# Optimization experiments

Measured on AMD Instinct MI355X. Metric: run time of the kernel, lower is better.

## Reference

```python
import jax, jax.numpy as jnp
import numpy as np

B, S, E, H = 4, 2048, 1024, 16
D = E // H  # head_dim = 64


def setup_inputs() -> dict:
    key = jax.random.key(0)
    k1, k2, k3 = jax.random.split(key, 3)
    x = jax.random.normal(k1, (B, S, E), dtype=jnp.float32)
    w_attn = jax.random.normal(k2, (E, 3 * E), dtype=jnp.float32) * (E ** -0.5)
    b_attn = jnp.zeros((3 * E,), dtype=jnp.float32)
    w_out = jax.random.normal(k3, (E, E), dtype=jnp.float32) * (E ** -0.5)
    b_out = jnp.zeros((E,), dtype=jnp.float32)
    return {"x": x, "w_attn": w_attn, "b_attn": b_attn, "w_out": w_out, "b_out": b_out}


def reference(x, w_attn, b_attn, w_out, b_out):
    b, s, e = x.shape
    qkv = x @ w_attn + b_attn                      # [b, s, 3e]
    q, k, v = jnp.split(qkv, 3, axis=2)
    q = q.reshape(b, s, H, D)
    k = k.reshape(b, s, H, D)
    v = v.reshape(b, s, H, D)
    energy = jnp.einsum('nqhd,nkhd->nhqk', q, k)   # [b, H, s, s]
    causal = jnp.tril(jnp.ones((s, s), dtype=bool))
    energy = jnp.where(causal, energy, -jnp.inf)
    scale = jnp.sqrt(jnp.float32(D))
    attn = jax.nn.softmax(energy / scale, axis=-1)  # dropout_rate=0.0 -> identity
    out = jnp.einsum('nhql,nlhd->nqhd', attn, v).reshape(b, s, e)
    return out @ w_out + b_out
```

## Files before the change

### kernel.cpp

```cpp
#include <hip/hip_runtime.h>

typedef short bf16x8 __attribute__((ext_vector_type(8)));
typedef float f32x4 __attribute__((ext_vector_type(4)));
typedef float f32x16 __attribute__((ext_vector_type(16)));
typedef float float4v __attribute__((ext_vector_type(4)));
typedef short short4v __attribute__((ext_vector_type(4)));
typedef unsigned uint2v __attribute__((ext_vector_type(2)));
typedef unsigned uint4v __attribute__((ext_vector_type(4)));

#define B_ 4
#define S_ 2048
#define E_ 1024
#define H_ 16
#define D_ 64
#define M_ (B_*S_)
#define N1_ (3*E_)

__device__ inline short f2bs(float f) {
    unsigned u = __builtin_bit_cast(unsigned, f);
    unsigned r = u + 0x7fffu + ((u >> 16) & 1u);
    return (short)(r >> 16);
}
__device__ inline float exp2a(float x) {
    float r; asm("v_exp_f32 %0, %1" : "=v"(r) : "v"(x)); return r;
}
__device__ inline unsigned cvtpk(float a, float b) {
    unsigned r; asm("v_cvt_pk_bf16_f32 %0, %1, %2" : "=v"(r) : "v"(a), "v"(b)); return r;
}

__device__ inline const __attribute__((address_space(1))) void* gas(const void* p) {
    return (const __attribute__((address_space(1))) void*)p;
}
__device__ inline __attribute__((address_space(3))) void* las(void* p) {
    return (__attribute__((address_space(3))) void*)p;
}

__global__ void convert_f32_bf16(const float* __restrict__ in, short* __restrict__ out, int n) {
    int tid = blockIdx.x * blockDim.x + threadIdx.x;
    int stride = gridDim.x * blockDim.x;
    for (int i = tid * 4; i < n; i += stride * 4) {
        float4v v = *(const float4v*)&in[i];
        short4v o;
        o[0] = f2bs(v[0]); o[1] = f2bs(v[1]); o[2] = f2bs(v[2]); o[3] = f2bs(v[3]);
        *(short4v*)&out[i] = o;
    }
}

__global__ void transpose_convert(const float* __restrict__ in, short* __restrict__ out,
                                  int rows, int cols) {
    __shared__ float t[32][33];
    int bx = blockIdx.x * 32;
    int by = blockIdx.y * 32;
    int tx = threadIdx.x, ty = threadIdx.y;
#pragma unroll
    for (int i = 0; i < 4; ++i)
        t[ty + i * 8][tx] = in[(size_t)(by + ty + i * 8) * cols + bx + tx];
    __syncthreads();
#pragma unroll
    for (int i = 0; i < 4; ++i)
        out[(size_t)(bx + ty + i * 8) * rows + by + tx] = f2bs(t[tx][ty + i * 8]);
}

#define MFMA16(Q) \
    _Pragma("unroll") for (int mf = 0; mf < 2; ++mf) \
    _Pragma("unroll") for (int nf = 0; nf < 4; ++nf) { \
        acc[(Q)*2+mf][nf] = __builtin_amdgcn_mfma_f32_16x16x32_bf16(af[mf][0], bfrag[nf][0], acc[(Q)*2+mf][nf], 0, 0, 0); \
        acc[(Q)*2+mf][nf] = __builtin_amdgcn_mfma_f32_16x16x32_bf16(af[mf][1], bfrag[nf][1], acc[(Q)*2+mf][nf], 0, 0, 0); \
    }

#define PHASE(Q, STAGE_STMT, WAITV) do { \
    bf16x8 af[2][2]; \
    _Pragma("unroll") for (int mf = 0; mf < 2; ++mf) \
    _Pragma("unroll") for (int ks = 0; ks < 2; ++ks) { \
        int r = (Q)*32 + mf*16 + li; \
        af[mf][ks] = *(const bf16x8*)(lA + r*128 + ((ks*64 + g*16) ^ ((r & 7) << 4))); \
    } \
    STAGE_STMT; \
    __builtin_amdgcn_s_barrier(); \
    asm volatile("s_waitcnt lgkmcnt(0)" ::: "memory"); \
    __builtin_amdgcn_sched_barrier(0); \
    __builtin_amdgcn_s_setprio(1); \
    MFMA16(Q); \
    __builtin_amdgcn_s_setprio(0); \
    WAITV; \
    __builtin_amdgcn_s_barrier(); \
} while (0)

#define VMW(n) asm volatile("s_waitcnt vmcnt(" #n ")" ::: "memory")
#define NOP_ ((void)0)

__global__ __launch_bounds__(512, 2) void gemm256_qkv(
    const short* __restrict__ A, const short* __restrict__ Bt,
    const float* __restrict__ bias,
    short* __restrict__ Qb, short* __restrict__ Kb, short* __restrict__ Vt) {
    __shared__ __attribute__((aligned(16))) short lds[2][2][2][8192];
    const int tid = threadIdx.x;
    const int lane = tid & 63;
    const int wid = tid >> 6;
    const int li = lane & 15, g = lane >> 4;
    const int wr = wid >> 2, wc = wid & 3;
    const int Kdim = E_;
    const int NT = Kdim >> 6;

    const int id = blockIdx.x;
    const int swz = (id & 7) * 48 + (id >> 3);
    const int bx = swz % 12, by = swz / 12;
    const int row0 = by * 256, col0 = bx * 256;

    const int rstage = wid * 8 + (lane >> 3);
    const int cstage = (((lane & 7) ^ ((lane >> 3) & 7)) << 4);

    auto stageA = [&](int buf, int kt, int seg) {
#pragma unroll
        for (int h = 0; h < 2; ++h) {
            const char* src = (const char*)A +
                ((size_t)(row0 + h * 128 + seg * 64 + rstage) * Kdim + kt * 64) * 2 + cstage;
            char* dst = (char*)&lds[buf][0][h][0] + seg * 8192 + wid * 1024;
            __builtin_amdgcn_global_load_lds(gas(src), las(dst), 16, 0, 0);
        }
    };
    auto stageB = [&](int buf, int kt, int h) {
#pragma unroll
        for (int seg = 0; seg < 2; ++seg) {
            const char* src = (const char*)Bt +
                ((size_t)(col0 + h * 128 + seg * 64 + rstage) * Kdim + kt * 64) * 2 + cstage;
            char* dst = (char*)&lds[buf][1][h][0] + seg * 8192 + wid * 1024;
            __builtin_amdgcn_global_load_lds(gas(src), las(dst), 16, 0, 0);
        }
    };

    f32x4 acc[8][4];
#pragma unroll
    for (int m = 0; m < 8; ++m)
#pragma unroll
        for (int n = 0; n < 4; ++n) acc[m][n] = (f32x4){0.f, 0.f, 0.f, 0.f};

    stageB(0, 0, 0);
    stageB(0, 0, 1);
    stageA(0, 0, 0);
    stageA(0, 0, 1);
    asm volatile("s_waitcnt vmcnt(0)" ::: "memory");
    __syncthreads();

    const int bc = (wc & 1) * 64;
    for (int t = 0; t < NT; ++t) {
        const int cur = t & 1;
        const int nb = cur ^ 1;
        const int tn = t + 1;
        const bool st = (tn < NT);
        const char* lA = (const char*)&lds[cur][0][wr][0];
        const char* lB = (const char*)&lds[cur][1][wc >> 1][0];

        bf16x8 bfrag[4][2];
#pragma unroll
        for (int nf = 0; nf < 4; ++nf)
#pragma unroll
            for (int ks = 0; ks < 2; ++ks) {
                int r = bc + nf * 16 + li;
                bfrag[nf][ks] = *(const bf16x8*)(lB + r * 128 + ((ks * 64 + g * 16) ^ ((r & 7) << 4)));
            }
        if (st) {
            PHASE(0, stageB(nb, tn, 0), NOP_);
            PHASE(1, stageB(nb, tn, 1), VMW(4));
            PHASE(2, stageA(nb, tn, 0), NOP_);
            PHASE(3, stageA(nb, tn, 1), VMW(2));
        } else {
            PHASE(0, NOP_, NOP_);
            PHASE(1, NOP_, VMW(0));
            PHASE(2, NOP_, NOP_);
            PHASE(3, NOP_, NOP_);
        }
    }

    if (col0 < 2048) {
        short* Dst = (col0 < 1024) ? Qb : Kb;
#pragma unroll
        for (int nf = 0; nf < 4; ++nf) {
            int ncolg = col0 + wc * 64 + nf * 16 + li;
            float bv = bias[ncolg];
            int ncol = ncolg & 1023;
#pragma unroll
            for (int mi = 0; mi < 8; ++mi) {
                int rbase = row0 + wr * 128 + mi * 16 + 4 * g;
#pragma unroll
                for (int j = 0; j < 4; ++j)
                    Dst[(size_t)(rbase + j) * E_ + ncol] = f2bs(acc[mi][nf][j] + bv);
            }
        }
    } else {
#pragma unroll
        for (int nf = 0; nf < 4; ++nf) {
            int ncolg = col0 + wc * 64 + nf * 16 + li;
            float bv = bias[ncolg];
            int rem = ncolg & 1023;
            int h = rem >> 6, d = rem & 63;
#pragma unroll
            for (int mi = 0; mi < 8; ++mi) {
                int s0 = row0 + wr * 128 + mi * 16 + 4 * g;
                int bb2 = s0 >> 11;
                int ss = s0 & 2047;
                uint2v p;
                p[0] = cvtpk(acc[mi][nf][0] + bv, acc[mi][nf][1] + bv);
                p[1] = cvtpk(acc[mi][nf][2] + bv, acc[mi][nf][3] + bv);
                *(uint2v*)&Vt[((size_t)(bb2 * H_ + h) * D_ + d) * S_ + ss] = p;
            }
        }
    }
}

__global__ __launch_bounds__(256, 2) void gemm_bt_out(
    const short* __restrict__ A, const short* __restrict__ Bt,
    const float* __restrict__ bias, float* __restrict__ Cf,
    int Kdim, int Ndim) {
    __shared__ __attribute__((aligned(16))) short As[128 * 32];
    __shared__ __attribute__((aligned(16))) short Bs[128 * 32];
    const int lane = threadIdx.x & 63;
    const int wv = threadIdx.x >> 6;
    const int row0 = blockIdx.y * 128;
    const int col0 = blockIdx.x * 128;
    const int wr = (wv >> 1) * 64;
    const int wc = (wv & 1) * 64;
    const int li = lane & 15;
    const int g = lane >> 4;
    const int lr = lane >> 2;
    const int lk = (lane & 3) * 8;

    f32x4 acc[4][4];
#pragma unroll
    for (int m = 0; m < 4; ++m)
#pragma unroll
        for (int n = 0; n < 4; ++n) acc[m][n] = (f32x4){0.f, 0.f, 0.f, 0.f};

    for (int k0 = 0; k0 < Kdim; k0 += 32) {
#pragma unroll
        for (int i = 0; i < 2; ++i) {
            int cc = wv * 2 + i;
            const short* ga = A + (size_t)(row0 + cc * 16 + lr) * Kdim + k0 + lk;
            __builtin_amdgcn_global_load_lds(gas(ga), las(&As[cc * 512]), 16, 0, 0);
            const short* gb = Bt + (size_t)(col0 + cc * 16 + lr) * Kdim + k0 + lk;
            __builtin_amdgcn_global_load_lds(gas(gb), las(&Bs[cc * 512]), 16, 0, 0);
        }
        __syncthreads();
        bf16x8 af[4], bfr[4];
#pragma unroll
        for (int m = 0; m < 4; ++m) af[m] = *(const bf16x8*)&As[(wr + 16 * m + li) * 32 + g * 8];
#pragma unroll
        for (int n = 0; n < 4; ++n) bfr[n] = *(const bf16x8*)&Bs[(wc + 16 * n + li) * 32 + g * 8];
#pragma unroll
        for (int m = 0; m < 4; ++m)
#pragma unroll
            for (int n = 0; n < 4; ++n)
                acc[m][n] = __builtin_amdgcn_mfma_f32_16x16x32_bf16(af[m], bfr[n], acc[m][n], 0, 0, 0);
        __syncthreads();
    }

#pragma unroll
    for (int n = 0; n < 4; ++n) {
        int ncol = col0 + wc + 16 * n + li;
        float bv = bias[ncol];
#pragma unroll
        for (int m = 0; m < 4; ++m) {
            int rbase = row0 + wr + 16 * m + 4 * g;
#pragma unroll
            for (int j = 0; j < 4; ++j)
                Cf[(size_t)(rbase + j) * Ndim + ncol] = acc[m][n][j] + bv;
        }
    }
}

__global__ __launch_bounds__(256, 4) void attn_kernel(
    const short* __restrict__ Qb, const short* __restrict__ Kb,
    const short* __restrict__ Vt, short* __restrict__ Ob) {
    __shared__ __attribute__((aligned(16))) short Kl[4096];
    __shared__ __attribute__((aligned(16))) short Vl[4096];
    const int lane = threadIdx.x & 63;
    const int wv = threadIdx.x >> 6;
    const int l31 = lane & 31;
    const int hi = lane >> 5;
    const int id = blockIdx.x;
    const int xcd = id & 7;
    const int r_ = id >> 3;
    const int qt = 15 - (r_ >> 3);
    const int bh = xcd * 8 + (r_ & 7);
    const int bb = bh >> 4, hh = bh & 15;
    const short* Qh = Qb + (size_t)bb * (S_ * E_) + hh * 64;
    const short* Kh = Kb + (size_t)bb * (S_ * E_) + hh * 64;
    const short* Vh = Vt + (size_t)bh * (D_ * S_);
    const float CEXP = 0.18033688011112042f;

    const int rstage = wv * 8 + (lane >> 3);
    const int cstage = (((lane & 7) ^ ((lane >> 3) & 7)) << 4);

    const int q0w = qt * 128 + wv * 32;
    const int q = q0w + l31;

    bf16x8 qf[4];
#pragma unroll
    for (int c = 0; c < 4; ++c)
        qf[c] = *(const bf16x8*)&Qh[(size_t)q * E_ + c * 16 + hi * 8];

    f32x16 acc[2];
#pragma unroll
    for (int d = 0; d < 2; ++d)
#pragma unroll
        for (int r = 0; r < 16; ++r) acc[d][r] = 0.f;
    float m = -3e38f, mC = 0.f, l = 0.f;

    const int nw = (q0w + 95) >> 6;
    const int nt = (qt * 128 + 191) >> 6;

    for (int it = 0; it < nt; ++it) {
        const int kt0 = it * 64;
#pragma unroll
        for (int half = 0; half < 2; ++half) {
            const char* gk = (const char*)(Kh + (size_t)(kt0 + half * 32 + rstage) * E_) + cstage;
            __builtin_amdgcn_global_load_lds(gas(gk), las((char*)Kl + half * 4096 + wv * 1024), 16, 0, 0);
            const char* gv = (const char*)Vh + (size_t)(half * 32 + rstage) * (S_ * 2) + (size_t)kt0 * 2 + cstage;
            __builtin_amdgcn_global_load_lds(gas(gv), las((char*)Vl + half * 4096 + wv * 1024), 16, 0, 0);
        }
        __syncthreads();
        if (it < nw) {
            f32x16 sc0, sc1;
#pragma unroll
            for (int r = 0; r < 16; ++r) { sc0[r] = 0.f; sc1[r] = 0.f; }
#pragma unroll
            for (int c = 0; c < 4; ++c) {
                const int r0 = l31, r1 = 32 + l31;
                bf16x8 kf0 = *(const bf16x8*)((const char*)Kl + r0 * 128 +
                                              ((c * 32 + hi * 16) ^ ((r0 & 7) << 4)));
                bf16x8 kf1 = *(const bf16x8*)((const char*)Kl + r1 * 128 +
                                              ((c * 32 + hi * 16) ^ ((r1 & 7) << 4)));
                sc0 = __builtin_amdgcn_mfma_f32_32x32x16_bf16(kf0, qf[c], sc0, 0, 0, 0);
                sc1 = __builtin_amdgcn_mfma_f32_32x32x16_bf16(kf1, qf[c], sc1, 0, 0, 0);
            }
            if (kt0 + 63 > q0w) {
                const int kb = kt0 + 4 * hi;
#pragma unroll
                for (int r = 0; r < 16; ++r) {
                    int key = kb + (r & 3) + 8 * (r >> 2);
                    sc0[r] = (key > q) ? -3e38f : sc0[r];
                    sc1[r] = (key + 32 > q) ? -3e38f : sc1[r];
                }
            }
            float tmx[8];
#pragma unroll
            for (int r = 0; r < 8; ++r)
                tmx[r] = fmaxf(fmaxf(sc0[2 * r], sc0[2 * r + 1]),
                               fmaxf(sc1[2 * r], sc1[2 * r + 1]));
            float tm = fmaxf(fmaxf(fmaxf(tmx[0], tmx[1]), fmaxf(tmx[2], tmx[3])),
                             fmaxf(fmaxf(tmx[4], tmx[5]), fmaxf(tmx[6], tmx[7])));
            tm = fmaxf(tm, __shfl_xor(tm, 32, 64));
            bool need = (tm > m + 16.0f);
            if (__ballot((int)need) != 0ull) {
                float mn = fmaxf(m, tm);
                float sf = exp2a((m - mn) * CEXP);
                m = mn; mC = mn * CEXP;
                l *= sf;
#pragma unroll
                for (int d = 0; d < 2; ++d)
#pragma unroll
                    for (int r = 0; r < 16; ++r) acc[d][r] *= sf;
            }
#pragma unroll
            for (int r = 0; r < 16; ++r) {
                sc0[r] = exp2a(fmaf(sc0[r], CEXP, -mC));
                sc1[r] = exp2a(fmaf(sc1[r], CEXP, -mC));
            }
            float s0 = 0.f, s1 = 0.f;
#pragma unroll
            for (int r = 0; r < 8; ++r) {
                s0 += sc0[2 * r] + sc0[2 * r + 1];
                s1 += sc1[2 * r] + sc1[2 * r + 1];
            }
            float ls = s0 + s1;
            ls += __shfl_xor(ls, 32, 64);
            l += ls;
            const bool lo = (hi == 0);
            bf16x8 pf[4];
#pragma unroll
            for (int s = 0; s < 2; ++s) {
                const f32x16& p = s ? sc1 : sc0;
                unsigned W0 = cvtpk(p[0], p[1]),   W1 = cvtpk(p[2], p[3]);
                unsigned W2 = cvtpk(p[4], p[5]),   W3 = cvtpk(p[6], p[7]);
                unsigned W4 = cvtpk(p[8], p[9]),   W5 = cvtpk(p[10], p[11]);
                unsigned W6 = cvtpk(p[12], p[13]), W7 = cvtpk(p[14], p[15]);
                unsigned xW0 = __shfl_xor(W0, 32, 64), xW1 = __shfl_xor(W1, 32, 64);
                unsigned xW2 = __shfl_xor(W2, 32, 64), xW3 = __shfl_xor(W3, 32, 64);
                unsigned xW4 = __shfl_xor(W4, 32, 64), xW5 = __shfl_xor(W5, 32, 64);
                unsigned xW6 = __shfl_xor(W6, 32, 64), xW7 = __shfl_xor(W7, 32, 64);
                uint4v u1, u2;
                u1[0] = lo ? W0 : xW2;  u1[1] = lo ? W1 : xW3;
                u1[2] = lo ? xW0 : W2;  u1[3] = lo ? xW1 : W3;
                u2[0] = lo ? W4 : xW6;  u2[1] = lo ? W5 : xW7;
                u2[2] = lo ? xW4 : W6;  u2[3] = lo ? xW5 : W7;
                pf[s * 2] = __builtin_bit_cast(bf16x8, u1);
                pf[s * 2 + 1] = __builtin_bit_cast(bf16x8, u2);
            }
#pragma unroll
            for (int db = 0; db < 2; ++db) {
                const int row = db * 32 + l31;
                const int rsw = (row & 7) << 4;
                const char* vrow = (const char*)Vl + row * 128;
                bf16x8 v0 = *(const bf16x8*)(vrow + ((hi * 16) ^ rsw));
                bf16x8 v1 = *(const bf16x8*)(vrow + ((32 + hi * 16) ^ rsw));
                bf16x8 v2 = *(const bf16x8*)(vrow + ((64 + hi * 16) ^ rsw));
                bf16x8 v3 = *(const bf16x8*)(vrow + ((96 + hi * 16) ^ rsw));
                acc[db] = __builtin_amdgcn_mfma_f32_32x32x16_bf16(v0, pf[0], acc[db], 0, 0, 0);
                acc[db] = __builtin_amdgcn_mfma_f32_32x32x16_bf16(v1, pf[1], acc[db], 0, 0, 0);
                acc[db] = __builtin_amdgcn_mfma_f32_32x32x16_bf16(v2, pf[2], acc[db], 0, 0, 0);
                acc[db] = __builtin_amdgcn_mfma_f32_32x32x16_bf16(v3, pf[3], acc[db], 0, 0, 0);
            }
        }
        __syncthreads();
    }

    float rl = __builtin_amdgcn_rcpf(l);
    short* orow = Ob + ((size_t)(bb * S_ + q)) * E_ + hh * 64;
#pragma unroll
    for (int db = 0; db < 2; ++db)
#pragma unroll
        for (int rb = 0; rb < 4; ++rb) {
            uint2v pk;
            pk[0] = cvtpk(acc[db][rb * 4 + 0] * rl, acc[db][rb * 4 + 1] * rl);
            pk[1] = cvtpk(acc[db][rb * 4 + 2] * rl, acc[db][rb * 4 + 3] * rl);
            *(uint2v*)&orow[db * 32 + rb * 8 + hi * 4] = pk;
        }
}

extern "C" void kernel_launch(void* const* d_in, const int* in_sizes, int n_in,
                              void* d_out, int out_size, void* d_ws, size_t ws_size,
                              hipStream_t stream) {
    const float* x      = (const float*)d_in[0];
    const float* w_attn = (const float*)d_in[1];
    const float* b_attn = (const float*)d_in[2];
    const float* w_out  = (const float*)d_in[3];
    const float* b_out  = (const float*)d_in[4];
    float* out = (float*)d_out;

    char* ws = (char*)d_ws;
    short* Xbf  = (short*)(ws);
    short* Wat  = (short*)(ws + (16ull << 20));
    short* Wot  = (short*)(ws + (22ull << 20));
    short* Qb   = (short*)(ws + (24ull << 20));
    short* Kb   = (short*)(ws + (40ull << 20));
    short* Vt   = (short*)(ws + (56ull << 20));
    short* Obuf = Xbf;

    convert_f32_bf16<<<2048, 256, 0, stream>>>(x, Xbf, M_ * E_);
    transpose_convert<<<dim3(N1_ / 32, E_ / 32), dim3(32, 8), 0, stream>>>(w_attn, Wat, E_, N1_);
    transpose_convert<<<dim3(E_ / 32, E_ / 32), dim3(32, 8), 0, stream>>>(w_out, Wot, E_, E_);

    gemm256_qkv<<<384, 512, 0, stream>>>(Xbf, Wat, b_attn, Qb, Kb, Vt);

    attn_kernel<<<1024, 256, 0, stream>>>(Qb, Kb, Vt, Obuf);

    gemm_bt_out<<<dim3(E_ / 128, M_ / 128), 256, 0, stream>>>(
        Obuf, Wot, b_out, out, E_, E_);
}
```

Measured before the change: 177.0 us.

## Narrow QKV GEMM tiles to 256x128 and double-buffer K/V in attention

The QKV projection GEMM now uses 256x128 output tiles, launching 768 blocks instead of 384 and halving the B-tile LDS footprint and the accumulator registers per thread. The loads are regrouped across the four pipeline phases to match. The attention kernel now double-buffers its K and V LDS tiles, prefetching the next key block while the current one is computed, to hide global load latency. The trade-offs are more LDS in attention, which may limit occupancy, and lower arithmetic intensity per GEMM block.

Measured after the change: 192.3 us. +8.6%, slower.

```diff
diff --git a/kernel.cpp b/kernel.cpp
--- a/kernel.cpp
+++ b/kernel.cpp
@@ -61,9 +61,9 @@
         out[(size_t)(bx + ty + i * 8) * rows + by + tx] = f2bs(t[tx][ty + i * 8]);
 }
 
-#define MFMA16(Q) \
+#define MFMA8(Q) \
     _Pragma("unroll") for (int mf = 0; mf < 2; ++mf) \
-    _Pragma("unroll") for (int nf = 0; nf < 4; ++nf) { \
+    _Pragma("unroll") for (int nf = 0; nf < 2; ++nf) { \
         acc[(Q)*2+mf][nf] = __builtin_amdgcn_mfma_f32_16x16x32_bf16(af[mf][0], bfrag[nf][0], acc[(Q)*2+mf][nf], 0, 0, 0); \
         acc[(Q)*2+mf][nf] = __builtin_amdgcn_mfma_f32_16x16x32_bf16(af[mf][1], bfrag[nf][1], acc[(Q)*2+mf][nf], 0, 0, 0); \
     }
@@ -80,7 +80,7 @@
     asm volatile("s_waitcnt lgkmcnt(0)" ::: "memory"); \
     __builtin_amdgcn_sched_barrier(0); \
     __builtin_amdgcn_s_setprio(1); \
-    MFMA16(Q); \
+    MFMA8(Q); \
     __builtin_amdgcn_s_setprio(0); \
     WAITV; \
     __builtin_amdgcn_s_barrier(); \
@@ -89,11 +89,12 @@
 #define VMW(n) asm volatile("s_waitcnt vmcnt(" #n ")" ::: "memory")
 #define NOP_ ((void)0)
 
-__global__ __launch_bounds__(512, 2) void gemm256_qkv(
+__global__ __launch_bounds__(512, 2) void gemm_qkv(
     const short* __restrict__ A, const short* __restrict__ Bt,
     const float* __restrict__ bias,
     short* __restrict__ Qb, short* __restrict__ Kb, short* __restrict__ Vt) {
-    __shared__ __attribute__((aligned(16))) short lds[2][2][2][8192];
+    __shared__ __attribute__((aligned(16))) short ldsA[2][2][2][4096];
+    __shared__ __attribute__((aligned(16))) short ldsB[2][8192];
     const int tid = threadIdx.x;
     const int lane = tid & 63;
     const int wid = tid >> 6;
@@ -103,9 +104,9 @@
     const int NT = Kdim >> 6;
 
     const int id = blockIdx.x;
-    const int swz = (id & 7) * 48 + (id >> 3);
-    const int bx = swz % 12, by = swz / 12;
-    const int row0 = by * 256, col0 = bx * 256;
+    const int swz = (id & 7) * 96 + (id >> 3);
+    const int bx = swz % 24, by = swz / 24;
+    const int row0 = by * 256, col0 = bx * 128;
 
     const int rstage = wid * 8 + (lane >> 3);
     const int cstage = (((lane & 7) ^ ((lane >> 3) & 7)) << 4);
@@ -115,55 +116,53 @@
         for (int h = 0; h < 2; ++h) {
             const char* src = (const char*)A +
                 ((size_t)(row0 + h * 128 + seg * 64 + rstage) * Kdim + kt * 64) * 2 + cstage;
-            char* dst = (char*)&lds[buf][0][h][0] + seg * 8192 + wid * 1024;
+            char* dst = (char*)&ldsA[buf][h][seg][0] + wid * 1024;
             __builtin_amdgcn_global_load_lds(gas(src), las(dst), 16, 0, 0);
         }
     };
-    auto stageB = [&](int buf, int kt, int h) {
-#pragma unroll
-        for (int seg = 0; seg < 2; ++seg) {
+    auto stageB = [&](int buf, int kt) {
+#pragma unroll
+        for (int i = 0; i < 2; ++i) {
             const char* src = (const char*)Bt +
-                ((size_t)(col0 + h * 128 + seg * 64 + rstage) * Kdim + kt * 64) * 2 + cstage;
-            char* dst = (char*)&lds[buf][1][h][0] + seg * 8192 + wid * 1024;
+                ((size_t)(col0 + i * 64 + rstage) * Kdim + kt * 64) * 2 + cstage;
+            char* dst = (char*)&ldsB[buf][0] + i * 8192 + wid * 1024;
             __builtin_amdgcn_global_load_lds(gas(src), las(dst), 16, 0, 0);
         }
     };
 
-    f32x4 acc[8][4];
+    f32x4 acc[8][2];
 #pragma unroll
     for (int m = 0; m < 8; ++m)
 #pragma unroll
-        for (int n = 0; n < 4; ++n) acc[m][n] = (f32x4){0.f, 0.f, 0.f, 0.f};
-
-    stageB(0, 0, 0);
-    stageB(0, 0, 1);
+        for (int n = 0; n < 2; ++n) acc[m][n] = (f32x4){0.f, 0.f, 0.f, 0.f};
+
+    stageB(0, 0);
     stageA(0, 0, 0);
     stageA(0, 0, 1);
     asm volatile("s_waitcnt vmcnt(0)" ::: "memory");
     __syncthreads();
 
-    const int bc = (wc & 1) * 64;
     for (int t = 0; t < NT; ++t) {
         const int cur = t & 1;
         const int nb = cur ^ 1;
         const int tn = t + 1;
         const bool st = (tn < NT);
-        const char* lA = (const char*)&lds[cur][0][wr][0];
-        const char* lB = (const char*)&lds[cur][1][wc >> 1][0];
-
-        bf16x8 bfrag[4][2];
-#pragma unroll
-        for (int nf = 0; nf < 4; ++nf)
+        const char* lA = (const char*)&ldsA[cur][wr][0][0];
+        const char* lB = (const char*)&ldsB[cur][0];
+
+        bf16x8 bfrag[2][2];
+#pragma unroll
+        for (int nf = 0; nf < 2; ++nf)
 #pragma unroll
             for (int ks = 0; ks < 2; ++ks) {
-                int r = bc + nf * 16 + li;
+                int r = wc * 32 + nf * 16 + li;
                 bfrag[nf][ks] = *(const bf16x8*)(lB + r * 128 + ((ks * 64 + g * 16) ^ ((r & 7) << 4)));
             }
         if (st) {
-            PHASE(0, stageB(nb, tn, 0), NOP_);
-            PHASE(1, stageB(nb, tn, 1), VMW(4));
-            PHASE(2, stageA(nb, tn, 0), NOP_);
-            PHASE(3, stageA(nb, tn, 1), VMW(2));
+            PHASE(0, stageB(nb, tn), NOP_);
+            PHASE(1, stageA(nb, tn, 0), VMW(4));
+            PHASE(2, stageA(nb, tn, 1), NOP_);
+            PHASE(3, NOP_, VMW(2));
         } else {
             PHASE(0, NOP_, NOP_);
             PHASE(1, NOP_, VMW(0));
@@ -175,8 +174,8 @@
     if (col0 < 2048) {
         short* Dst = (col0 < 1024) ? Qb : Kb;
 #pragma unroll
-        for (int nf = 0; nf < 4; ++nf) {
-            int ncolg = col0 + wc * 64 + nf * 16 + li;
+        for (int nf = 0; nf < 2; ++nf) {
+            int ncolg = col0 + wc * 32 + nf * 16 + li;
             float bv = bias[ncolg];
             int ncol = ncolg & 1023;
 #pragma unroll
@@ -189,8 +188,8 @@
         }
     } else {
 #pragma unroll
-        for (int nf = 0; nf < 4; ++nf) {
-            int ncolg = col0 + wc * 64 + nf * 16 + li;
+        for (int nf = 0; nf < 2; ++nf) {
+            int ncolg = col0 + wc * 32 + nf * 16 + li;
             float bv = bias[ncolg];
             int rem = ncolg & 1023;
             int h = rem >> 6, d = rem & 63;
@@ -271,8 +270,8 @@
 __global__ __launch_bounds__(256, 4) void attn_kernel(
     const short* __restrict__ Qb, const short* __restrict__ Kb,
     const short* __restrict__ Vt, short* __restrict__ Ob) {
-    __shared__ __attribute__((aligned(16))) short Kl[4096];
-    __shared__ __attribute__((aligned(16))) short Vl[4096];
+    __shared__ __attribute__((aligned(16))) short Kl[2][4096];
+    __shared__ __attribute__((aligned(16))) short Vl[2][4096];
     const int lane = threadIdx.x & 63;
     const int wv = threadIdx.x >> 6;
     const int l31 = lane & 31;
@@ -309,27 +308,35 @@
     const int nw = (q0w + 95) >> 6;
     const int nt = (qt * 128 + 191) >> 6;
 
-    for (int it = 0; it < nt; ++it) {
+    auto stage = [&](int it, int buf) {
         const int kt0 = it * 64;
 #pragma unroll
         for (int half = 0; half < 2; ++half) {
             const char* gk = (const char*)(Kh + (size_t)(kt0 + half * 32 + rstage) * E_) + cstage;
-            __builtin_amdgcn_global_load_lds(gas(gk), las((char*)Kl + half * 4096 + wv * 1024), 16, 0, 0);
+            __builtin_amdgcn_global_load_lds(gas(gk), las((char*)&Kl[buf][0] + half * 4096 + wv * 1024), 16, 0, 0);
             const char* gv = (const char*)Vh + (size_t)(half * 32 + rstage) * (S_ * 2) + (size_t)kt0 * 2 + cstage;
-            __builtin_amdgcn_global_load_lds(gas(gv), las((char*)Vl + half * 4096 + wv * 1024), 16, 0, 0);
-        }
-        __syncthreads();
+            __builtin_amdgcn_global_load_lds(gas(gv), las((char*)&Vl[buf][0] + half * 4096 + wv * 1024), 16, 0, 0);
+        }
+    };
+
+    stage(0, 0);
+    __syncthreads();
+
+    for (int it = 0; it < nt; ++it) {
+        const int buf = it & 1;
+        if (it + 1 < nt) stage(it + 1, buf ^ 1);
         if (it < nw) {
+            const int kt0 = it * 64;
+            const char* Kb_ = (const char*)&Kl[buf][0];
+            const char* Vb_ = (const char*)&Vl[buf][0];
             f32x16 sc0, sc1;
 #pragma unroll
             for (int r = 0; r < 16; ++r) { sc0[r] = 0.f; sc1[r] = 0.f; }
 #pragma unroll
             for (int c = 0; c < 4; ++c) {
                 const int r0 = l31, r1 = 32 + l31;
-                bf16x8 kf0 = *(const bf16x8*)((const char*)Kl + r0 * 128 +
-                                              ((c * 32 + hi * 16) ^ ((r0 & 7) << 4)));
-                bf16x8 kf1 = *(const bf16x8*)((const char*)Kl + r1 * 128 +
-                                              ((c * 32 + hi * 16) ^ ((r1 & 7) << 4)));
+                bf16x8 kf0 = *(const bf16x8*)(Kb_ + r0 * 128 + ((c * 32 + hi * 16) ^ ((r0 & 7) << 4)));
+                bf16x8 kf1 = *(const bf16x8*)(Kb_ + r1 * 128 + ((c * 32 + hi * 16) ^ ((r1 & 7) << 4)));
                 sc0 = __builtin_amdgcn_mfma_f32_32x32x16_bf16(kf0, qf[c], sc0, 0, 0, 0);
                 sc1 = __builtin_amdgcn_mfma_f32_32x32x16_bf16(kf1, qf[c], sc1, 0, 0, 0);
             }
@@ -400,7 +407,7 @@
             for (int db = 0; db < 2; ++db) {
                 const int row = db * 32 + l31;
                 const int rsw = (row & 7) << 4;
-                const char* vrow = (const char*)Vl + row * 128;
+                const char* vrow = Vb_ + row * 128;
                 bf16x8 v0 = *(const bf16x8*)(vrow + ((hi * 16) ^ rsw));
                 bf16x8 v1 = *(const bf16x8*)(vrow + ((32 + hi * 16) ^ rsw));
                 bf16x8 v2 = *(const bf16x8*)(vrow + ((64 + hi * 16) ^ rsw));
@@ -450,7 +457,7 @@
     transpose_convert<<<dim3(N1_ / 32, E_ / 32), dim3(32, 8), 0, stream>>>(w_attn, Wat, E_, N1_);
     transpose_convert<<<dim3(E_ / 32, E_ / 32), dim3(32, 8), 0, stream>>>(w_out, Wot, E_, E_);
 
-    gemm256_qkv<<<384, 512, 0, stream>>>(Xbf, Wat, b_attn, Qb, Kb, Vt);
+    gemm_qkv<<<768, 512, 0, stream>>>(Xbf, Wat, b_attn, Qb, Kb, Vt);
 
     attn_kernel<<<1024, 256, 0, stream>>>(Qb, Kb, Vt, Obuf);
 
```
